# Kernel optimization log

Hardware: AMD Instinct MI355X
Metric: run time of the kernel (lower is better)

## Reference

```python
import jax, jax.numpy as jnp
import numpy as np
from jax import lax
from functools import partial

MAX_FRAMES = 12
NUM_SAMPLES = 500
SIGMA = 0.05
TOPK = 49
LN_EPS = 1e-5


def perturbed_topk_indicators(scores, noise, k):
    """scores: (b, d), noise: (b, ns, d) -> indicators (b, k, d).
    Equivalent to one_hot(sorted_topk_indices).mean(samples) without
    materializing the (b, ns, k, d) one-hot tensor (histogram scatter)."""
    b, ns, d = noise.shape
    perturbed = scores[:, None, :] + SIGMA * noise          # (b, ns, d)
    _, idx = lax.top_k(perturbed, k)                        # (b, ns, k)
    idx = jnp.sort(idx, axis=-1)                            # ascending, as in torch code
    # scatter-add counts into (b, k, d)
    flat = (jnp.arange(b)[:, None, None] * k + jnp.arange(k)[None, None, :]) * d + idx
    counts = jnp.zeros(b * k * d, scores.dtype).at[flat.ravel()].add(1.0)
    return counts.reshape(b, k, d) / ns


def reference(x, ln_w, ln_b, w_in, w_out1, w_out2):
    B, L, D = x.shape
    N = L // MAX_FRAMES
    xf = x.reshape(B * MAX_FRAMES, N, D)                    # (Bf, N, D)
    Bf = B * MAX_FRAMES

    # ---- STPredictorConv ----
    mu = xf.mean(-1, keepdims=True)
    var = jnp.var(xf, axis=-1, keepdims=True)
    xn = (xf - mu) * lax.rsqrt(var + LN_EPS) * ln_w + ln_b
    h = jax.nn.gelu(jnp.einsum('bnd,cd->bnc', xn, w_in), approximate=False)  # (Bf, N, C=256)
    C = h.shape[-1]
    g = h[:, :1, :].reshape(B, MAX_FRAMES, 1, C).mean(axis=1, keepdims=True)  # (B,1,1,C)
    g = jnp.broadcast_to(g, (B, MAX_FRAMES, 1, C)).reshape(Bf, 1, C)
    cat = jnp.concatenate([h, jnp.broadcast_to(g, (Bf, N, C))], axis=-1)      # (Bf, N, 2C)
    s = jax.nn.gelu(jnp.einsum('bnd,cd->bnc', cat, w_out1), approximate=False)
    s = jnp.einsum('bnc,oc->bno', s, w_out2)                # (Bf, N, 1)
    score = jax.nn.softmax(s, axis=-1)[..., 0]              # softmax over size-1 dim -> ones; faithful

    # ---- perturbed top-k selection over spatial tokens ----
    spatial_score = score[:, 1:]                            # (Bf, N-1)
    noise = jax.random.normal(jax.random.key(42), (Bf, NUM_SAMPLES, N - 1), x.dtype)
    ind = perturbed_topk_indicators(spatial_score, noise, TOPK)  # (Bf, k, N-1)

    cls_feat = xf[:, :1, :]
    spatial_feat = xf[:, 1:, :]
    selected = jnp.einsum('bkl,bld->bkd', ind, spatial_feat)
    out = jnp.concatenate([cls_feat, selected], axis=1)     # (Bf, 1+k, D)
    return out.reshape(B, MAX_FRAMES * (1 + TOPK), D)


def setup_inputs() -> dict:
    key = jax.random.key(0)
    ks = jax.random.split(key, 4)
    B, N, D, C = 8, 197, 512, 256
    x = jax.random.normal(ks[0], (B, MAX_FRAMES * N, D), jnp.float32)
    return {
        'x': x,
        'ln_w': jnp.ones((D,), jnp.float32),
        'ln_b': jnp.zeros((D,), jnp.float32),
        'w_in': jax.random.normal(ks[1], (C, D), jnp.float32) * 0.02,
        'w_out1': jax.random.normal(ks[2], (C, D), jnp.float32) * 0.02,
        'w_out2': jax.random.normal(ks[3], (1, C), jnp.float32) * 0.02,
    }
```

## Files before the change

kernel.cpp:

```cpp
#include <hip/hip_runtime.h>
#include <stdint.h>

constexpr int BF   = 96;
constexpr int NS   = 500;
constexpr int DSP  = 196;
constexpr int KSEL = 49;
constexpr int NTOK = 197;
constexpr int DIM  = 512;
constexpr int ROWSTRIDE = 64;

__device__ __forceinline__ uint32_t rotl32(uint32_t x, int r) {
  return __builtin_amdgcn_alignbit(x, x, 32 - r);
}

__device__ __forceinline__ void threefry2x32(uint32_t x0, uint32_t x1,
                                             uint32_t& o0, uint32_t& o1) {
  const uint32_t ks0 = 0u, ks1 = 42u, ks2 = 0u ^ 42u ^ 0x1BD11BDAu;
  x0 += ks0; x1 += ks1;
#define TF_R(r) { x0 += x1; x1 = rotl32(x1, (r)); x1 ^= x0; }
  TF_R(13) TF_R(15) TF_R(26) TF_R(6)   x0 += ks1; x1 += ks2 + 1u;
  TF_R(17) TF_R(29) TF_R(16) TF_R(24)  x0 += ks2; x1 += ks0 + 2u;
  TF_R(13) TF_R(15) TF_R(26) TF_R(6)   x0 += ks0; x1 += ks1 + 3u;
  TF_R(17) TF_R(29) TF_R(16) TF_R(24)  x0 += ks1; x1 += ks2 + 4u;
  TF_R(13) TF_R(15) TF_R(26) TF_R(6)   x0 += ks2; x1 += ks0 + 5u;
#undef TF_R
  o0 = x0; o1 = x1;
}

__device__ __forceinline__ uint32_t noise_bits(uint32_t p) {
  uint32_t o0, o1;
  threefry2x32(0u, p, o0, o1);
  return o0 ^ o1;
}

__global__ __launch_bounds__(256)
void topk_idx_kernel(uint8_t* __restrict__ idxbuf) {
  const int lane = threadIdx.x & 63;
  const int wid  = (blockIdx.x << 2) | (threadIdx.x >> 6);
  const uint32_t rowbase = (uint32_t)wid * (uint32_t)DSP;

  uint32_t m[4];
#pragma unroll
  for (int g = 0; g < 4; ++g) {
    const int j = (g << 6) | lane;
    uint32_t v = 0u;
    if (j < DSP) v = noise_bits(rowbase + (uint32_t)j) >> 9;
    m[g] = v;
  }

  uint32_t T = 0u;
#pragma unroll 1
  for (int bit = 22; bit >= 0; --bit) {
    const uint32_t cand = T | (1u << bit);
    const int c = __popcll(__ballot(m[0] >= cand))
                + __popcll(__ballot(m[1] >= cand))
                + __popcll(__ballot(m[2] >= cand))
                + __popcll(__ballot(m[3] >= cand));
    if (c >= KSEL) T = cand;
  }

  uint64_t gt[4], eq[4];
#pragma unroll
  for (int g = 0; g < 4; ++g) {
    gt[g] = __ballot(m[g] > T);
    eq[g] = __ballot(m[g] == T);
  }
  eq[3] &= 0xFull;

  const int ngt = __popcll(gt[0]) + __popcll(gt[1]) + __popcll(gt[2]) + __popcll(gt[3]);
  const int need = KSEL - ngt;
  const int e0 = __popcll(eq[0]), e1 = __popcll(eq[1]), e2 = __popcll(eq[2]);
  const uint64_t below = (1ull << lane) - 1ull;

  uint64_t fin[4];
  fin[0] = gt[0] | __ballot(((eq[0] >> lane) & 1ull) &&
                            (__popcll(eq[0] & below) < need));
  fin[1] = gt[1] | __ballot(((eq[1] >> lane) & 1ull) &&
                            (e0 + __popcll(eq[1] & below) < need));
  fin[2] = gt[2] | __ballot(((eq[2] >> lane) & 1ull) &&
                            (e0 + e1 + __popcll(eq[2] & below) < need));
  fin[3] = gt[3] | __ballot(((eq[3] >> lane) & 1ull) &&
                            (e0 + e1 + e2 + __popcll(eq[3] & below) < need));

  const int c0 = __popcll(fin[0]);
  const int c1 = c0 + __popcll(fin[1]);
  const int c2 = c1 + __popcll(fin[2]);

  uint8_t* row = idxbuf + (size_t)wid * ROWSTRIDE;
  if ((fin[0] >> lane) & 1ull) row[__popcll(fin[0] & below)]      = (uint8_t)lane;
  if ((fin[1] >> lane) & 1ull) row[c0 + __popcll(fin[1] & below)] = (uint8_t)(64 + lane);
  if ((fin[2] >> lane) & 1ull) row[c1 + __popcll(fin[2] & below)] = (uint8_t)(128 + lane);
  if ((fin[3] >> lane) & 1ull) row[c2 + __popcll(fin[3] & below)] = (uint8_t)(192 + lane);
}

__global__ __launch_bounds__(512)
void hist_kernel(const float* __restrict__ x,
                 const uint8_t* __restrict__ idxbuf,
                 uint16_t* __restrict__ cnt,
                 float* __restrict__ out) {
  const int b = blockIdx.x;
  const int t = threadIdx.x;

  __shared__ uint32_t hist[KSEL * DSP];
  for (int i = t; i < KSEL * DSP; i += 512) hist[i] = 0u;
  __syncthreads();

  const uint32_t* rows = (const uint32_t*)(idxbuf + (size_t)b * NS * ROWSTRIDE);
  for (int c = t; c < NS * 4; c += 512) {
    const int s = c >> 2, part = c & 3;
    const uint4 v = *(const uint4*)(rows + s * 16 + part * 4);
    if (part < 3) {
      const int kbase = part * 16;
#pragma unroll
      for (int q = 0; q < 4; ++q) {
        uint32_t w = (&v.x)[q];
#pragma unroll
        for (int bb = 0; bb < 4; ++bb) {
          atomicAdd(&hist[(kbase + q * 4 + bb) * DSP + (w & 0xffu)], 1u);
          w >>= 8;
        }
      }
    } else {
      atomicAdd(&hist[48 * DSP + (v.x & 0xffu)], 1u);
    }
  }
  __syncthreads();

  uint16_t* cb = cnt + (size_t)b * KSEL * DSP;
  for (int i = t; i < KSEL * DSP; i += 512) cb[i] = (uint16_t)hist[i];

  out[(size_t)b * (1 + KSEL) * DIM + t] = x[(size_t)b * NTOK * DIM + t];
}

__global__ __launch_bounds__(256)
void gemm_kernel(const float* __restrict__ x,
                 const uint16_t* __restrict__ cnt,
                 float* __restrict__ out) {
  const int b = blockIdx.x % BF;
  const int dtile = blockIdx.x / BF;
  const int t = threadIdx.x;
  const int dt = t & 15, kg = t >> 4;

  constexpr int JP = DSP / 2;
  __shared__ uint32_t cfp[64 * JP];
  const uint32_t* cp = (const uint32_t*)(cnt + (size_t)b * KSEL * DSP);
  for (int i = t; i < KSEL * JP; i += 256) cfp[i] = cp[i];
  for (int i = KSEL * JP + t; i < 64 * JP; i += 256) cfp[i] = 0u;
  __syncthreads();

  const float* xb = x + (size_t)b * NTOK * DIM + DIM
                  + dtile * 64 + dt * 4;
  float4 acc[4] = {};
#pragma unroll 2
  for (int j2 = 0; j2 < JP; ++j2) {
    const float4 xv0 = *(const float4*)(xb + (size_t)(2 * j2) * DIM);
    const float4 xv1 = *(const float4*)(xb + (size_t)(2 * j2 + 1) * DIM);
#pragma unroll
    for (int i = 0; i < 4; ++i) {
      const uint32_t pr = cfp[(kg + 16 * i) * JP + j2];
      const float c0 = (float)(pr & 0xffffu);
      const float c1 = (float)(pr >> 16);
      acc[i].x = fmaf(c0, xv0.x, acc[i].x);
      acc[i].y = fmaf(c0, xv0.y, acc[i].y);
      acc[i].z = fmaf(c0, xv0.z, acc[i].z);
      acc[i].w = fmaf(c0, xv0.w, acc[i].w);
      acc[i].x = fmaf(c1, xv1.x, acc[i].x);
      acc[i].y = fmaf(c1, xv1.y, acc[i].y);
      acc[i].z = fmaf(c1, xv1.z, acc[i].z);
      acc[i].w = fmaf(c1, xv1.w, acc[i].w);
    }
  }

  float* ob = out + (size_t)b * (1 + KSEL) * DIM + dtile * 64 + dt * 4;
  const float inv = 1.0f / (float)NS;
#pragma unroll
  for (int i = 0; i < 4; ++i) {
    const int k = kg + 16 * i;
    if (k < KSEL) {
      float4 r;
      r.x = acc[i].x * inv; r.y = acc[i].y * inv;
      r.z = acc[i].z * inv; r.w = acc[i].w * inv;
      *(float4*)(ob + (size_t)(1 + k) * DIM) = r;
    }
  }
}

extern "C" void kernel_launch(void* const* d_in, const int* in_sizes, int n_in,
                              void* d_out, int out_size, void* d_ws, size_t ws_size,
                              hipStream_t stream) {
  const float* x = (const float*)d_in[0];
  float* out = (float*)d_out;
  uint8_t* idxbuf = (uint8_t*)d_ws;
  uint16_t* cnt = (uint16_t*)((uint8_t*)d_ws +
                              (size_t)BF * NS * ROWSTRIDE);

  topk_idx_kernel<<<dim3(BF * NS / 4), 256, 0, stream>>>(idxbuf);
  hist_kernel<<<dim3(BF), 512, 0, stream>>>(x, idxbuf, cnt, out);
  gemm_kernel<<<dim3(BF * 8), 256, 0, stream>>>(x, cnt, out);
}
```

Before: 146.1 us.

## Split histogram by rank groups and GEMM by k-halves for more blocks

The histogram kernel is split into 7 blocks per frame, each counting 8 ranks, instead of one block per frame handling all 49 ranks in a large shared histogram. The GEMM kernel is split into two k-halves per d-tile, doubling its block count and halving its per-block accumulator work. The CLS-token copy moves from the histogram kernel into the GEMM kernel. The aim is to fill the GPU with more blocks and cut per-block LDS footprint. The cost is repeated idx loads and some redundant work, since rank 24 is computed twice and the last rank group reads padding bytes.

```diff
diff --git a/kernel.cpp b/kernel.cpp
--- a/kernel.cpp
+++ b/kernel.cpp
@@ -93,43 +93,37 @@
   if ((fin[3] >> lane) & 1ull) row[c2 + __popcll(fin[3] & below)] = (uint8_t)(192 + lane);
 }
 
-__global__ __launch_bounds__(512)
-void hist_kernel(const float* __restrict__ x,
-                 const uint8_t* __restrict__ idxbuf,
-                 uint16_t* __restrict__ cnt,
-                 float* __restrict__ out) {
-  const int b = blockIdx.x;
+__global__ __launch_bounds__(256)
+void hist_kernel(const uint8_t* __restrict__ idxbuf,
+                 uint16_t* __restrict__ cnt) {
+  const int b = blockIdx.x % BF;
+  const int g = blockIdx.x / BF;
   const int t = threadIdx.x;
 
-  __shared__ uint32_t hist[KSEL * DSP];
-  for (int i = t; i < KSEL * DSP; i += 512) hist[i] = 0u;
+  __shared__ uint32_t hist[8 * DSP];
+  for (int i = t; i < 8 * DSP; i += 256) hist[i] = 0u;
   __syncthreads();
 
-  const uint32_t* rows = (const uint32_t*)(idxbuf + (size_t)b * NS * ROWSTRIDE);
-  for (int c = t; c < NS * 4; c += 512) {
-    const int s = c >> 2, part = c & 3;
-    const uint4 v = *(const uint4*)(rows + s * 16 + part * 4);
-    if (part < 3) {
-      const int kbase = part * 16;
-#pragma unroll
-      for (int q = 0; q < 4; ++q) {
-        uint32_t w = (&v.x)[q];
-#pragma unroll
-        for (int bb = 0; bb < 4; ++bb) {
-          atomicAdd(&hist[(kbase + q * 4 + bb) * DSP + (w & 0xffu)], 1u);
-          w >>= 8;
-        }
+  const uint8_t* base = idxbuf + (size_t)b * NS * ROWSTRIDE + 8 * g;
+  for (int r = t; r < NS; r += 256) {
+    const uint2 v = *(const uint2*)(base + (size_t)r * ROWSTRIDE);
+#pragma unroll
+    for (int q = 0; q < 2; ++q) {
+      uint32_t w = q ? v.y : v.x;
+#pragma unroll
+      for (int bb = 0; bb < 4; ++bb) {
+        atomicAdd(&hist[(q * 4 + bb) * DSP + (w & 0xffu)], 1u);
+        w >>= 8;
       }
-    } else {
-      atomicAdd(&hist[48 * DSP + (v.x & 0xffu)], 1u);
     }
   }
   __syncthreads();
 
   uint16_t* cb = cnt + (size_t)b * KSEL * DSP;
-  for (int i = t; i < KSEL * DSP; i += 512) cb[i] = (uint16_t)hist[i];
-
-  out[(size_t)b * (1 + KSEL) * DIM + t] = x[(size_t)b * NTOK * DIM + t];
+  for (int i = t; i < 8 * DSP; i += 256) {
+    const int rank = 8 * g + i / DSP;
+    if (rank < KSEL) cb[(size_t)rank * DSP + (i % DSP)] = (uint16_t)hist[i];
+  }
 }
 
 __global__ __launch_bounds__(256)
@@ -137,26 +131,30 @@
                  const uint16_t* __restrict__ cnt,
                  float* __restrict__ out) {
   const int b = blockIdx.x % BF;
-  const int dtile = blockIdx.x / BF;
+  const int tmp = blockIdx.x / BF;
+  const int dtile = tmp & 7;
+  const int khalf = tmp >> 3;
+  const int k0 = khalf * 24;
   const int t = threadIdx.x;
   const int dt = t & 15, kg = t >> 4;
 
   constexpr int JP = DSP / 2;
-  __shared__ uint32_t cfp[64 * JP];
-  const uint32_t* cp = (const uint32_t*)(cnt + (size_t)b * KSEL * DSP);
-  for (int i = t; i < KSEL * JP; i += 256) cfp[i] = cp[i];
-  for (int i = KSEL * JP + t; i < 64 * JP; i += 256) cfp[i] = 0u;
+  __shared__ uint32_t cfp[32 * JP];
+  const uint32_t* cp = (const uint32_t*)(cnt + (size_t)b * KSEL * DSP)
+                     + (size_t)k0 * JP;
+  for (int i = t; i < 25 * JP; i += 256) cfp[i] = cp[i];
+  for (int i = 25 * JP + t; i < 32 * JP; i += 256) cfp[i] = 0u;
   __syncthreads();
 
   const float* xb = x + (size_t)b * NTOK * DIM + DIM
                   + dtile * 64 + dt * 4;
-  float4 acc[4] = {};
+  float4 acc[2] = {};
 #pragma unroll 2
   for (int j2 = 0; j2 < JP; ++j2) {
     const float4 xv0 = *(const float4*)(xb + (size_t)(2 * j2) * DIM);
     const float4 xv1 = *(const float4*)(xb + (size_t)(2 * j2 + 1) * DIM);
 #pragma unroll
-    for (int i = 0; i < 4; ++i) {
+    for (int i = 0; i < 2; ++i) {
       const uint32_t pr = cfp[(kg + 16 * i) * JP + j2];
       const float c0 = (float)(pr & 0xffffu);
       const float c1 = (float)(pr >> 16);
@@ -174,14 +172,21 @@
   float* ob = out + (size_t)b * (1 + KSEL) * DIM + dtile * 64 + dt * 4;
   const float inv = 1.0f / (float)NS;
 #pragma unroll
-  for (int i = 0; i < 4; ++i) {
-    const int k = kg + 16 * i;
-    if (k < KSEL) {
+  for (int i = 0; i < 2; ++i) {
+    const int kl = kg + 16 * i;
+    const int k = k0 + kl;
+    if (kl < 25 && k < KSEL) {
       float4 r;
       r.x = acc[i].x * inv; r.y = acc[i].y * inv;
       r.z = acc[i].z * inv; r.w = acc[i].w * inv;
       *(float4*)(ob + (size_t)(1 + k) * DIM) = r;
     }
+  }
+
+  if (khalf == 0 && kg == 0) {
+    const float4 c4 = *(const float4*)(x + (size_t)b * NTOK * DIM
+                                       + dtile * 64 + dt * 4);
+    *(float4*)(ob) = c4;
   }
 }
 
@@ -195,6 +200,6 @@
                               (size_t)BF * NS * ROWSTRIDE);
 
   topk_idx_kernel<<<dim3(BF * NS / 4), 256, 0, stream>>>(idxbuf);
-  hist_kernel<<<dim3(BF), 512, 0, stream>>>(x, idxbuf, cnt, out);
-  gemm_kernel<<<dim3(BF * 8), 256, 0, stream>>>(x, cnt, out);
-}
+  hist_kernel<<<dim3(BF * 7), 256, 0, stream>>>(idxbuf, cnt);
+  gemm_kernel<<<dim3(BF * 8 * 2), 256, 0, stream>>>(x, cnt, out);
+}
```

New measurement: 165.5 us. 1.13x slower.
